# Kernel optimization log

Measured on AMD Instinct MI355X. Metric: run time of the kernel, lower is better.

The kernel has to match this reference:

```python
import jax, jax.numpy as jnp
import numpy as np

B, S, D, H = 2, 2048, 1024, 16
HD = D // H
EPS = 1e-5


def setup_inputs() -> dict:
    key = jax.random.key(0)
    ks = jax.random.split(key, 12)
    n = lambda k, shp, s=0.02: jax.random.normal(k, shp, dtype=jnp.float32) * s
    return {
        "x": jax.random.normal(ks[0], (B, S, D), dtype=jnp.float32),
        "Wq": n(ks[1], (D, D)), "bq": jnp.zeros((D,), jnp.float32),
        "Wk": n(ks[2], (D, D)), "bk": jnp.zeros((D,), jnp.float32),
        "Wv": n(ks[3], (D, D)), "bv": jnp.zeros((D,), jnp.float32),
        "Wo": n(ks[4], (D, D)), "bo": jnp.zeros((D,), jnp.float32),
        "rel_bias": n(ks[5], (H, S, S)),  # relative_position_bias param (window==S)
        "gamma": jnp.ones((D,), jnp.float32),
        "beta": jnp.zeros((D,), jnp.float32),
    }


def reference(x, Wq, bq, Wk, bk, Wv, bv, Wo, bo, rel_bias, gamma, beta):
    b, s, d = x.shape
    # projections (torch Linear: x @ W.T + b), split heads -> (b, h, s, hd)
    def proj(W, bias):
        return (x @ W.T + bias).reshape(b, s, H, HD).transpose(0, 2, 1, 3)
    Q, K, V = proj(Wq, bq), proj(Wk, bk), proj(Wv, bv)

    scores = jnp.einsum("bhqd,bhkd->bhqk", Q, K) / jnp.sqrt(jnp.float32(HD))
    # additive causal mask (-inf strictly above diagonal) + relative position bias
    i = jnp.arange(s)
    causal = jnp.where(i[:, None] >= i[None, :], 0.0, -jnp.inf).astype(scores.dtype)
    scores = scores + causal[None, None] + rel_bias[None, :, :s, :s]

    attn = jax.nn.softmax(scores, axis=-1)  # dropout is identity in eval mode
    attended = jnp.einsum("bhqk,bhkd->bhqd", attn, V)
    attended = attended.transpose(0, 2, 1, 3).reshape(b, s, d)

    out = attended @ Wo.T + bo
    # residual + LayerNorm(eps=1e-5)
    y = out + x
    mu = jnp.mean(y, axis=-1, keepdims=True)
    var = jnp.var(y, axis=-1, keepdims=True)
    return (y - mu) / jnp.sqrt(var + EPS) * gamma + beta
```

## Files before the change

kernel.cpp:

```cpp
#include <hip/hip_runtime.h>

typedef __attribute__((ext_vector_type(8))) short short8;
typedef __attribute__((ext_vector_type(4))) float f32x4;
typedef unsigned short u16;
typedef __attribute__((ext_vector_type(4))) unsigned short u16x4;

#define S_LEN 2048
#define DMODEL 1024
#define NH 16
#define HD 64

static __device__ __forceinline__ u16 f2bf(float f) {
    union { float f; unsigned u; } x; x.f = f;
    unsigned r = x.u + 0x7fffu + ((x.u >> 16) & 1u);
    return (u16)(r >> 16);
}

static __device__ __forceinline__ unsigned cvtpk_bf16(float lo, float hi) {
    unsigned r;
    asm("v_cvt_pk_bf16_f32 %0, %1, %2" : "=v"(r) : "v"(lo), "v"(hi));
    return r;
}

#define GLD_LDS16(g, l) __builtin_amdgcn_global_load_lds( \
    (const __attribute__((address_space(1))) void*)(g),   \
    (__attribute__((address_space(3))) void*)(l), 16, 0, 0)

#define MFMA16(a, b, c) __builtin_amdgcn_mfma_f32_16x16x32_bf16(a, b, c, 0, 0, 0)

#define LOAD_FENCE() asm volatile("" ::: "memory")

#define TILE_SYNC() do {                                          \
    asm volatile("s_waitcnt vmcnt(4)" ::: "memory");              \
    __builtin_amdgcn_s_barrier();                                 \
    __builtin_amdgcn_sched_barrier(0);                            \
} while (0)

#define TILE_SYNC_FULL() do {                                     \
    asm volatile("s_waitcnt vmcnt(0)" ::: "memory");              \
    __builtin_amdgcn_s_barrier();                                 \
    __builtin_amdgcn_sched_barrier(0);                            \
} while (0)

__global__ __launch_bounds__(256) void cast_kernel(const float* __restrict__ in,
                                                   u16* __restrict__ out, int n4) {
    int i = blockIdx.x * 256 + threadIdx.x;
    if (i < n4) {
        const float4 v = reinterpret_cast<const float4*>(in)[i];
        u16x4 o;
        o.x = f2bf(v.x); o.y = f2bf(v.y); o.z = f2bf(v.z); o.w = f2bf(v.w);
        reinterpret_cast<u16x4*>(out)[i] = o;
    }
}

__global__ __launch_bounds__(256) void cast4_kernel(
    const float* __restrict__ w0, const float* __restrict__ w1,
    const float* __restrict__ w2, const float* __restrict__ w3,
    u16* __restrict__ o0, u16* __restrict__ o1,
    u16* __restrict__ o2, u16* __restrict__ o3, int n4) {
    const int z = blockIdx.y;
    const float* in = (z == 0) ? w0 : (z == 1) ? w1 : (z == 2) ? w2 : w3;
    u16* out = (z == 0) ? o0 : (z == 1) ? o1 : (z == 2) ? o2 : o3;
    int i = blockIdx.x * 256 + threadIdx.x;
    if (i < n4) {
        const float4 v = reinterpret_cast<const float4*>(in)[i];
        u16x4 o;
        o.x = f2bf(v.x); o.y = f2bf(v.y); o.z = f2bf(v.z); o.w = f2bf(v.w);
        reinterpret_cast<u16x4*>(out)[i] = o;
    }
}


#define GEMM_STAGE(SRC, SRCLD, KCOL, LDSBASE) do {                            \
    _Pragma("unroll")                                                          \
    for (int _i = 0; _i < 2; ++_i) {                                           \
        const int _s = _i * 256 + tid;                                         \
        const int _row = _s >> 2;                                              \
        const int _u = (_s & 3) ^ ((_row >> 1) & 3);                           \
        GLD_LDS16((SRC) + (size_t)(_row) * (SRCLD) + (KCOL) + _u * 8,          \
                  (LDSBASE) + _s * 8);                                         \
    }                                                                          \
} while (0)

static __device__ __forceinline__ short8 lds_frag(const u16* base, int row, int lg) {
    const int u = lg ^ ((row >> 1) & 3);
    return *(const short8*)(base + row * 32 + u * 8);
}

__global__ __launch_bounds__(256) void gemm_qkv_kernel(
    const u16* __restrict__ xbf,
    const u16* __restrict__ wqbf, const u16* __restrict__ wkbf, const u16* __restrict__ wvbf,
    const float* __restrict__ bq, const float* __restrict__ bk, const float* __restrict__ bv,
    u16* __restrict__ qout, u16* __restrict__ kout, u16* __restrict__ vtout)
{
    __shared__ u16 As[2][128][32];
    __shared__ u16 Bs[2][128][32];

    const int z = blockIdx.z;
    const u16* __restrict__ W = (z == 0) ? wqbf : (z == 1) ? wkbf : wvbf;
    const float* __restrict__ bias = (z == 0) ? bq : (z == 1) ? bk : bv;

    const int tid  = threadIdx.x;
    const int lane = tid & 63;
    const int wid  = tid >> 6;
    const int wm = (wid >> 1) * 64;
    const int wn = (wid & 1) * 64;
    const int lr = lane & 15;
    const int lg = lane >> 4;

    const int m0 = blockIdx.y * 128;
    const int n0 = blockIdx.x * 128;

    const u16* __restrict__ Abase = xbf + (size_t)m0 * DMODEL;
    const u16* __restrict__ Bbase = W + (size_t)n0 * DMODEL;

    f32x4 acc[4][4] = {};

#define QKV_COMPUTE(BUF)                                                      \
    do {                                                                      \
        short8 af[4], bfr[4];                                                 \
        _Pragma("unroll")                                                     \
        for (int t = 0; t < 4; ++t)                                           \
            af[t] = lds_frag(&As[BUF][0][0], wm + t * 16 + lr, lg);           \
        _Pragma("unroll")                                                     \
        for (int t = 0; t < 4; ++t)                                           \
            bfr[t] = lds_frag(&Bs[BUF][0][0], wn + t * 16 + lr, lg);          \
        _Pragma("unroll")                                                     \
        for (int mt = 0; mt < 4; ++mt)                                        \
            _Pragma("unroll")                                                 \
            for (int nt = 0; nt < 4; ++nt)                                    \
                acc[mt][nt] = MFMA16(af[mt], bfr[nt], acc[mt][nt]);           \
    } while (0)

    GEMM_STAGE(Abase, DMODEL, 0, &As[0][0][0]);
    GEMM_STAGE(Bbase, DMODEL, 0, &Bs[0][0][0]);
    __syncthreads();

    for (int kt = 0; kt < 32; kt += 2) {
        GEMM_STAGE(Abase, DMODEL, (kt + 1) * 32, &As[1][0][0]);
        GEMM_STAGE(Bbase, DMODEL, (kt + 1) * 32, &Bs[1][0][0]);
        LOAD_FENCE();
        QKV_COMPUTE(0);
        TILE_SYNC_FULL();

        if (kt + 2 < 32) {
            GEMM_STAGE(Abase, DMODEL, (kt + 2) * 32, &As[0][0][0]);
            GEMM_STAGE(Bbase, DMODEL, (kt + 2) * 32, &Bs[0][0][0]);
            LOAD_FENCE();
        }
        QKV_COMPUTE(1);
        TILE_SYNC_FULL();
    }
#undef QKV_COMPUTE

#pragma unroll
    for (int mt = 0; mt < 4; ++mt) {
#pragma unroll
        for (int nt = 0; nt < 4; ++nt) {
            const int n = n0 + wn + nt * 16 + lr;
            const int h = (n >> 6) & (NH - 1);
            const int hd = n & (HD - 1);
            const float bia = bias[n];
#pragma unroll
            for (int r = 0; r < 4; ++r) {
                const int m = m0 + wm + mt * 16 + lg * 4 + r;
                const int bb = m >> 11;
                const int ss = m & (S_LEN - 1);
                const float v = acc[mt][nt][r] + bia;
                const int bh = bb * NH + h;
                if (z == 0) {
                    qout[((size_t)bh * S_LEN + ss) * HD + hd] = f2bf(v * 0.125f);
                } else if (z == 1) {
                    kout[((size_t)bh * S_LEN + ss) * HD + hd] = f2bf(v);
                } else {
                    vtout[((size_t)bh * HD + hd) * S_LEN + ss] = f2bf(v);
                }
            }
        }
    }
}

__global__ __launch_bounds__(256, 3) void attn_kernel(
    const u16* __restrict__ qbf, const u16* __restrict__ kbf,
    const u16* __restrict__ vtbf, const float* __restrict__ rel,
    u16* __restrict__ att)
{
    __shared__ u16 Klds[2][64][64];
    __shared__ u16 Vlds[2][64][64];
    __shared__ u16 P[4][16][72];

    const int tid  = threadIdx.x;
    const int lane = tid & 63;
    const int wid  = tid >> 6;
    const int c = lane & 15;
    const int g = lane >> 4;

    const int h = blockIdx.x >> 1;
    const int b = blockIdx.x & 1;
    const int bh = b * NH + h;
    const int blkq = gridDim.y - 1 - blockIdx.y;
    const int q0 = blkq * 64;
    const int qv = q0 + wid * 16 + c;

    const size_t base = (size_t)bh * S_LEN * HD;

    const short8 qf0 = *(const short8*)&qbf[base + (size_t)qv * HD + g * 8];
    const short8 qf1 = *(const short8*)&qbf[base + (size_t)qv * HD + 32 + g * 8];

    const float* __restrict__ relrow = rel + (size_t)h * S_LEN * S_LEN + (size_t)qv * S_LEN;

    f32x4 o[4] = {};
    float m_run = -3e38f, l_run = 0.f;
    f32x4 rbA[4], rbB[4];

    const int nkt = blkq + 1;

    auto stage = [&](int kt, int bb) {
        const int k0 = kt * 64;
#pragma unroll
        for (int i = 0; i < 2; ++i) {
            const int s = i * 256 + tid;
            const int row = s >> 3;
            const int u = (s & 7) ^ (row & 7);
            GLD_LDS16(kbf + base + (size_t)(k0 + row) * HD + u * 8,
                      &Klds[bb][0][0] + s * 8);
        }
#pragma unroll
        for (int i = 0; i < 2; ++i) {
            const int s = i * 256 + tid;
            const int row = s >> 3;
            const int u = (s & 7) ^ (row & 7);
            GLD_LDS16(vtbf + base + (size_t)row * S_LEN + k0 + u * 8,
                      &Vlds[bb][0][0] + s * 8);
        }
    };

    auto rel_into = [&](f32x4 (&rb)[4], int kt) {
        const float* rn = relrow + kt * 64;
        rb[0] = *(const f32x4*)&rn[g * 4];
        rb[1] = *(const f32x4*)&rn[16 + g * 4];
        rb[2] = *(const f32x4*)&rn[32 + g * 4];
        rb[3] = *(const f32x4*)&rn[48 + g * 4];
    };

    auto compute_tile = [&](int cur, int k0, bool diag, const f32x4 (&rb)[4]) {
        short8 kf[8];
#pragma unroll
        for (int mt = 0; mt < 4; ++mt) {
            const u16* kp = &Klds[cur][0][0] + (mt * 16 + c) * 64;
            kf[2 * mt]     = *(const short8*)(kp + ((g ^ (c & 7)) * 8));
            kf[2 * mt + 1] = *(const short8*)(kp + (((4 + g) ^ (c & 7)) * 8));
        }
        f32x4 st[4] = {};
        __builtin_amdgcn_s_setprio(1);
#pragma unroll
        for (int mt = 0; mt < 4; ++mt) {
            st[mt] = MFMA16(kf[2 * mt], qf0, st[mt]);
            st[mt] = MFMA16(kf[2 * mt + 1], qf1, st[mt]);
        }
        __builtin_amdgcn_s_setprio(0);

        short8 vf[8];
#pragma unroll
        for (int nt = 0; nt < 4; ++nt) {
            const u16* vp = &Vlds[cur][0][0] + (nt * 16 + c) * 64;
            vf[2 * nt]     = *(const short8*)(vp + ((g ^ (c & 7)) * 8));
            vf[2 * nt + 1] = *(const short8*)(vp + (((4 + g) ^ (c & 7)) * 8));
        }

        float tm = -3e38f;
        if (diag) {
#pragma unroll
            for (int mt = 0; mt < 4; ++mt)
#pragma unroll
                for (int r = 0; r < 4; ++r) {
                    const int k = k0 + mt * 16 + g * 4 + r;
                    float sv = st[mt][r] + rb[mt][r];
                    if (k > qv) sv = -1e30f;
                    st[mt][r] = sv;
                    tm = fmaxf(tm, sv);
                }
        } else {
#pragma unroll
            for (int mt = 0; mt < 4; ++mt)
#pragma unroll
                for (int r = 0; r < 4; ++r) {
                    const float sv = st[mt][r] + rb[mt][r];
                    st[mt][r] = sv;
                    tm = fmaxf(tm, sv);
                }
        }

        if (!__all(tm <= m_run + 8.0f)) {
            tm = fmaxf(tm, __shfl_xor(tm, 16));
            tm = fmaxf(tm, __shfl_xor(tm, 32));
            const float mn = fmaxf(m_run, tm);
            const float sc = __expf(m_run - mn);
            m_run = mn;
            l_run *= sc;
#pragma unroll
            for (int r = 0; r < 4; ++r) {
                const float scq = __shfl(sc, g * 4 + r);
#pragma unroll
                for (int nt = 0; nt < 4; ++nt) o[nt][r] *= scq;
            }
        }

        float rsum = 0.f;
#pragma unroll
        for (int mt = 0; mt < 4; ++mt)
#pragma unroll
            for (int r = 0; r < 4; ++r) {
                const float e = __expf(st[mt][r] - m_run);
                st[mt][r] = e;
                rsum += e;
            }
        rsum += __shfl_xor(rsum, 16);
        rsum += __shfl_xor(rsum, 32);
        l_run += rsum;

#pragma unroll
        for (int mt = 0; mt < 4; ++mt) {
            uint2 pk;
            pk.x = cvtpk_bf16(st[mt][0], st[mt][1]);
            pk.y = cvtpk_bf16(st[mt][2], st[mt][3]);
            *(uint2*)&P[wid][c][mt * 16 + g * 4] = pk;
        }
        const short8 pa0 = *(const short8*)&P[wid][c][g * 8];
        const short8 pa1 = *(const short8*)&P[wid][c][32 + g * 8];

        __builtin_amdgcn_s_setprio(1);
        o[0] = MFMA16(pa0, vf[0], o[0]);
        o[0] = MFMA16(pa1, vf[1], o[0]);
        o[1] = MFMA16(pa0, vf[2], o[1]);
        o[1] = MFMA16(pa1, vf[3], o[1]);
        o[2] = MFMA16(pa0, vf[4], o[2]);
        o[2] = MFMA16(pa1, vf[5], o[2]);
        o[3] = MFMA16(pa0, vf[6], o[3]);
        o[3] = MFMA16(pa1, vf[7], o[3]);
        __builtin_amdgcn_s_setprio(0);
    };

    stage(0, 0);
    LOAD_FENCE();
    rel_into(rbA, 0);
    if (nkt > 1) rel_into(rbB, 1);
    __syncthreads();

    int cur = 0;
    int t = 0;
    while (t + 1 < nkt - 1) {
        stage(t + 1, cur ^ 1);
        LOAD_FENCE();
        compute_tile(cur, t * 64, false, rbA);
        rel_into(rbA, t + 2);
        LOAD_FENCE();
        TILE_SYNC();
        cur ^= 1;

        stage(t + 2, cur ^ 1);
        LOAD_FENCE();
        compute_tile(cur, (t + 1) * 64, false, rbB);
        if (t + 3 < nkt) {
            rel_into(rbB, t + 3);
            LOAD_FENCE();
            TILE_SYNC();
        } else {
            LOAD_FENCE();
            TILE_SYNC_FULL();
        }
        cur ^= 1;

        t += 2;
    }

    if (t < nkt - 1) {
        stage(t + 1, cur ^ 1);
        LOAD_FENCE();
        compute_tile(cur, t * 64, false, rbA);
        TILE_SYNC_FULL();
        cur ^= 1;
        compute_tile(cur, (nkt - 1) * 64, true, rbB);
    } else {
        compute_tile(cur, (nkt - 1) * 64, true, rbA);
    }

#pragma unroll
    for (int r = 0; r < 4; ++r) {
        const float linv = 1.0f / __shfl(l_run, g * 4 + r);
        const int q = q0 + wid * 16 + g * 4 + r;
#pragma unroll
        for (int nt = 0; nt < 4; ++nt) {
            att[((size_t)(b * S_LEN + q)) * DMODEL + h * HD + nt * 16 + c] =
                f2bf(o[nt][r] * linv);
        }
    }
}

__global__ __launch_bounds__(256) void gemm_o_kernel(
    const u16* __restrict__ att, const u16* __restrict__ wobf,
    const float* __restrict__ bo, const float* __restrict__ x,
    float* __restrict__ y)
{
    __shared__ u16 As[2][128][32];
    __shared__ u16 Bs[2][128][32];

    const int tid  = threadIdx.x;
    const int lane = tid & 63;
    const int wid  = tid >> 6;
    const int wm = (wid >> 1) * 64;
    const int wn = (wid & 1) * 64;
    const int lr = lane & 15;
    const int lg = lane >> 4;

    const int m0 = blockIdx.y * 128;
    const int n0 = blockIdx.x * 128;

    const u16* __restrict__ Abase = att + (size_t)m0 * DMODEL;
    const u16* __restrict__ Bbase = wobf + (size_t)n0 * DMODEL;

    f32x4 acc[4][4] = {};

#define O_COMPUTE(BUF)                                                        \
    do {                                                                      \
        short8 af[4], bfr[4];                                                 \
        _Pragma("unroll")                                                     \
        for (int t = 0; t < 4; ++t)                                           \
            af[t] = lds_frag(&As[BUF][0][0], wm + t * 16 + lr, lg);           \
        _Pragma("unroll")                                                     \
        for (int t = 0; t < 4; ++t)                                           \
            bfr[t] = lds_frag(&Bs[BUF][0][0], wn + t * 16 + lr, lg);          \
        _Pragma("unroll")                                                     \
        for (int mt = 0; mt < 4; ++mt)                                        \
            _Pragma("unroll")                                                 \
            for (int nt = 0; nt < 4; ++nt)                                    \
                acc[mt][nt] = MFMA16(af[mt], bfr[nt], acc[mt][nt]);           \
    } while (0)

    GEMM_STAGE(Abase, DMODEL, 0, &As[0][0][0]);
    GEMM_STAGE(Bbase, DMODEL, 0, &Bs[0][0][0]);
    __syncthreads();

    for (int kt = 0; kt < 32; kt += 2) {
        GEMM_STAGE(Abase, DMODEL, (kt + 1) * 32, &As[1][0][0]);
        GEMM_STAGE(Bbase, DMODEL, (kt + 1) * 32, &Bs[1][0][0]);
        LOAD_FENCE();
        O_COMPUTE(0);
        TILE_SYNC_FULL();

        if (kt + 2 < 32) {
            GEMM_STAGE(Abase, DMODEL, (kt + 2) * 32, &As[0][0][0]);
            GEMM_STAGE(Bbase, DMODEL, (kt + 2) * 32, &Bs[0][0][0]);
            LOAD_FENCE();
        }
        O_COMPUTE(1);
        TILE_SYNC_FULL();
    }
#undef O_COMPUTE

#pragma unroll
    for (int mt = 0; mt < 4; ++mt) {
#pragma unroll
        for (int nt = 0; nt < 4; ++nt) {
            const int n = n0 + wn + nt * 16 + lr;
            const float bia = bo[n];
#pragma unroll
            for (int r = 0; r < 4; ++r) {
                const int m = m0 + wm + mt * 16 + lg * 4 + r;
                const size_t idx = (size_t)m * DMODEL + n;
                y[idx] = acc[mt][nt][r] + bia + x[idx];
            }
        }
    }
}

__global__ __launch_bounds__(256) void ln_kernel(
    const float* __restrict__ y, const float* __restrict__ gamma,
    const float* __restrict__ beta, float* __restrict__ out)
{
    __shared__ float red[8];
    const int row = blockIdx.x;
    const int tid = threadIdx.x;
    const size_t base = (size_t)row * DMODEL + tid * 4;
    const float4 v = *(const float4*)&y[base];
    float s  = v.x + v.y + v.z + v.w;
    float ss = v.x * v.x + v.y * v.y + v.z * v.z + v.w * v.w;
#pragma unroll
    for (int off = 1; off < 64; off <<= 1) {
        s  += __shfl_xor(s, off);
        ss += __shfl_xor(ss, off);
    }
    const int w = tid >> 6;
    if ((tid & 63) == 0) { red[w] = s; red[4 + w] = ss; }
    __syncthreads();
    s  = red[0] + red[1] + red[2] + red[3];
    ss = red[4] + red[5] + red[6] + red[7];
    const float mu = s * (1.0f / DMODEL);
    const float var = ss * (1.0f / DMODEL) - mu * mu;
    const float rstd = rsqrtf(var + 1e-5f);
    const int col = tid * 4;
    float4 o;
    o.x = (v.x - mu) * rstd * gamma[col + 0] + beta[col + 0];
    o.y = (v.y - mu) * rstd * gamma[col + 1] + beta[col + 1];
    o.z = (v.z - mu) * rstd * gamma[col + 2] + beta[col + 2];
    o.w = (v.w - mu) * rstd * gamma[col + 3] + beta[col + 3];
    *(float4*)&out[base] = o;
}

extern "C" void kernel_launch(void* const* d_in, const int* in_sizes, int n_in,
                              void* d_out, int out_size, void* d_ws, size_t ws_size,
                              hipStream_t stream) {
    (void)in_sizes; (void)n_in; (void)out_size; (void)ws_size;
    const float* x     = (const float*)d_in[0];
    const float* Wq    = (const float*)d_in[1];
    const float* bq    = (const float*)d_in[2];
    const float* Wk    = (const float*)d_in[3];
    const float* bk    = (const float*)d_in[4];
    const float* Wv    = (const float*)d_in[5];
    const float* bv    = (const float*)d_in[6];
    const float* Wo    = (const float*)d_in[7];
    const float* bo    = (const float*)d_in[8];
    const float* rel   = (const float*)d_in[9];
    const float* gamma = (const float*)d_in[10];
    const float* beta  = (const float*)d_in[11];
    float* out = (float*)d_out;

    char* ws = (char*)d_ws;
    u16* xbf   = (u16*)(ws);
    u16* wqbf  = (u16*)(ws + ( 8u << 20));
    u16* wkbf  = (u16*)(ws + (10u << 20));
    u16* wvbf  = (u16*)(ws + (12u << 20));
    u16* wobf  = (u16*)(ws + (14u << 20));
    u16* qbf   = (u16*)(ws + (16u << 20));
    u16* kbf   = (u16*)(ws + (24u << 20));
    u16* vtbf  = (u16*)(ws + (32u << 20));
    u16* attbf = (u16*)(ws + (40u << 20));
    float* y   = (float*)(ws + (48u << 20));

    cast_kernel<<<4096, 256, 0, stream>>>(x, xbf, (2 * S_LEN * DMODEL) / 4);
    cast4_kernel<<<dim3(1024, 4), 256, 0, stream>>>(
        Wq, Wk, Wv, Wo, wqbf, wkbf, wvbf, wobf, (DMODEL * DMODEL) / 4);

    gemm_qkv_kernel<<<dim3(8, 32, 3), 256, 0, stream>>>(
        xbf, wqbf, wkbf, wvbf, bq, bk, bv, qbf, kbf, vtbf);

    attn_kernel<<<dim3(2 * NH, 32), 256, 0, stream>>>(qbf, kbf, vtbf, rel, attbf);

    gemm_o_kernel<<<dim3(8, 32), 256, 0, stream>>>(attbf, wobf, bo, x, y);

    ln_kernel<<<2 * S_LEN, 256, 0, stream>>>(y, gamma, beta, out);
}
```

Measured before the change: 172.1 us.

## Merge cast kernels, swizzle attention P buffer, raise attention occupancy bound

```diff
diff --git a/kernel.cpp b/kernel.cpp
--- a/kernel.cpp
+++ b/kernel.cpp
@@ -42,8 +42,22 @@
     __builtin_amdgcn_sched_barrier(0);                            \
 } while (0)
 
-__global__ __launch_bounds__(256) void cast_kernel(const float* __restrict__ in,
-                                                   u16* __restrict__ out, int n4) {
+__global__ __launch_bounds__(256) void cast_all_kernel(
+    const float* __restrict__ x,
+    const float* __restrict__ w0, const float* __restrict__ w1,
+    const float* __restrict__ w2, const float* __restrict__ w3,
+    u16* __restrict__ xo,
+    u16* __restrict__ o0, u16* __restrict__ o1,
+    u16* __restrict__ o2, u16* __restrict__ o3) {
+    const int z = blockIdx.y;
+    const int n4 = (DMODEL * DMODEL) / 4;
+    const float* in;
+    u16* out;
+    if (z < 4)      { in = x + (size_t)z * n4 * 4;  out = xo + (size_t)z * n4 * 4; }
+    else if (z == 4){ in = w0; out = o0; }
+    else if (z == 5){ in = w1; out = o1; }
+    else if (z == 6){ in = w2; out = o2; }
+    else            { in = w3; out = o3; }
     int i = blockIdx.x * 256 + threadIdx.x;
     if (i < n4) {
         const float4 v = reinterpret_cast<const float4*>(in)[i];
@@ -52,24 +66,6 @@
         reinterpret_cast<u16x4*>(out)[i] = o;
     }
 }
-
-__global__ __launch_bounds__(256) void cast4_kernel(
-    const float* __restrict__ w0, const float* __restrict__ w1,
-    const float* __restrict__ w2, const float* __restrict__ w3,
-    u16* __restrict__ o0, u16* __restrict__ o1,
-    u16* __restrict__ o2, u16* __restrict__ o3, int n4) {
-    const int z = blockIdx.y;
-    const float* in = (z == 0) ? w0 : (z == 1) ? w1 : (z == 2) ? w2 : w3;
-    u16* out = (z == 0) ? o0 : (z == 1) ? o1 : (z == 2) ? o2 : o3;
-    int i = blockIdx.x * 256 + threadIdx.x;
-    if (i < n4) {
-        const float4 v = reinterpret_cast<const float4*>(in)[i];
-        u16x4 o;
-        o.x = f2bf(v.x); o.y = f2bf(v.y); o.z = f2bf(v.z); o.w = f2bf(v.w);
-        reinterpret_cast<u16x4*>(out)[i] = o;
-    }
-}
-
 
 #define GEMM_STAGE(SRC, SRCLD, KCOL, LDSBASE) do {                            \
     _Pragma("unroll")                                                          \
@@ -180,14 +176,14 @@
     }
 }
 
-__global__ __launch_bounds__(256, 3) void attn_kernel(
+__global__ __launch_bounds__(256, 4) void attn_kernel(
     const u16* __restrict__ qbf, const u16* __restrict__ kbf,
     const u16* __restrict__ vtbf, const float* __restrict__ rel,
     u16* __restrict__ att)
 {
     __shared__ u16 Klds[2][64][64];
     __shared__ u16 Vlds[2][64][64];
-    __shared__ u16 P[4][16][72];
+    __shared__ u16 P[4][16][64];
 
     const int tid  = threadIdx.x;
     const int lane = tid & 63;
@@ -319,15 +315,17 @@
         rsum += __shfl_xor(rsum, 32);
         l_run += rsum;
 
+        char* prow = (char*)&P[wid][c][0];
 #pragma unroll
         for (int mt = 0; mt < 4; ++mt) {
             uint2 pk;
             pk.x = cvtpk_bf16(st[mt][0], st[mt][1]);
             pk.y = cvtpk_bf16(st[mt][2], st[mt][3]);
-            *(uint2*)&P[wid][c][mt * 16 + g * 4] = pk;
-        }
-        const short8 pa0 = *(const short8*)&P[wid][c][g * 8];
-        const short8 pa1 = *(const short8*)&P[wid][c][32 + g * 8];
+            const int gr = 2 * mt + (g >> 1);
+            *(uint2*)(prow + (((gr ^ (c & 7)) << 4) + ((g & 1) << 3))) = pk;
+        }
+        const short8 pa0 = *(const short8*)(prow + ((g ^ (c & 7)) << 4));
+        const short8 pa1 = *(const short8*)(prow + (((4 + g) ^ (c & 7)) << 4));
 
         __builtin_amdgcn_s_setprio(1);
         o[0] = MFMA16(pa0, vf[0], o[0]);
@@ -537,9 +535,8 @@
     u16* attbf = (u16*)(ws + (40u << 20));
     float* y   = (float*)(ws + (48u << 20));
 
-    cast_kernel<<<4096, 256, 0, stream>>>(x, xbf, (2 * S_LEN * DMODEL) / 4);
-    cast4_kernel<<<dim3(1024, 4), 256, 0, stream>>>(
-        Wq, Wk, Wv, Wo, wqbf, wkbf, wvbf, wobf, (DMODEL * DMODEL) / 4);
+    cast_all_kernel<<<dim3(1024, 8), 256, 0, stream>>>(
+        x, Wq, Wk, Wv, Wo, xbf, wqbf, wkbf, wvbf, wobf);
 
     gemm_qkv_kernel<<<dim3(8, 32, 3), 256, 0, stream>>>(
         xbf, wqbf, wkbf, wvbf, bq, bk, bv, qbf, kbf, vtbf);
```

Measured after the change: 292.0 us. 69.7% more time.
